# Kernel tuning notes

Measured on AMD Instinct MI355X. Metric: run time of the kernel, lower is better.

## Reference

```python
import jax, jax.numpy as jnp
import numpy as np

N_CLASSES = 18

def setup_inputs() -> dict:
    key = jax.random.key(0)
    k1, k2 = jax.random.split(key)
    B = 2_000_000
    output = jax.random.normal(k1, (B, N_CLASSES), dtype=jnp.float32)
    labels_soft = jax.random.uniform(k2, (B, N_CLASSES), dtype=jnp.float32)
    return {"output": output, "labels_soft": labels_soft}

def reference(output, labels_soft):
    # Original: sum over classes of mean_b( CE(output, cls) * labels_soft[:, cls] )
    # = mean over batch of sum_c( -log_softmax(output)[b, c] * labels_soft[b, c] )
    logp = jax.nn.log_softmax(output, axis=-1)          # [B, C]
    per_row = -jnp.sum(logp * labels_soft, axis=-1)     # [B]
    return jnp.mean(per_row)
```

## Files before the change

### kernel.cpp

```cpp
#include <hip/hip_runtime.h>

#define NCLS 18

__global__ __launch_bounds__(256) void ce_soft_kernel(
    const float* __restrict__ logits,
    const float* __restrict__ labels,
    float* __restrict__ result,
    int B, float invB)
{
    int tid = blockIdx.x * blockDim.x + threadIdx.x;
    int stride = gridDim.x * blockDim.x;

    float acc = 0.0f;
    for (int row = tid; row < B; row += stride) {
        const float2* o2 = (const float2*)(logits + (size_t)row * NCLS);
        const float2* l2 = (const float2*)(labels + (size_t)row * NCLS);
        float x[NCLS], l[NCLS];
        #pragma unroll
        for (int k = 0; k < NCLS / 2; ++k) {
            float2 v = o2[k];
            x[2 * k] = v.x; x[2 * k + 1] = v.y;
        }
        #pragma unroll
        for (int k = 0; k < NCLS / 2; ++k) {
            float2 w = l2[k];
            l[2 * k] = w.x; l[2 * k + 1] = w.y;
        }

        float m = x[0];
        #pragma unroll
        for (int c = 1; c < NCLS; ++c) m = fmaxf(m, x[c]);

        float se = 0.0f, dot = 0.0f, sl = 0.0f;
        #pragma unroll
        for (int c = 0; c < NCLS; ++c) {
            se += __expf(x[c] - m);
            dot = fmaf(l[c], x[c], dot);
            sl += l[c];
        }
        float lse = m + __logf(se);
        acc = fmaf(sl, lse, acc - dot);
    }

    #pragma unroll
    for (int off = 32; off > 0; off >>= 1)
        acc += __shfl_down(acc, off, 64);

    __shared__ float wave_sums[4];
    int lane = threadIdx.x & 63;
    int wid  = threadIdx.x >> 6;
    if (lane == 0) wave_sums[wid] = acc;
    __syncthreads();
    if (threadIdx.x == 0) {
        float s = wave_sums[0] + wave_sums[1] + wave_sums[2] + wave_sums[3];
        atomicAdd(result, s * invB);
    }
}

extern "C" void kernel_launch(void* const* d_in, const int* in_sizes, int n_in,
                              void* d_out, int out_size, void* d_ws, size_t ws_size,
                              hipStream_t stream) {
    const float* logits = (const float*)d_in[0];
    const float* labels = (const float*)d_in[1];
    float* result = (float*)d_out;

    int B = in_sizes[0] / NCLS;

    hipMemsetAsync(d_out, 0, sizeof(float), stream);

    int block = 256;
    int grid  = 2048;
    ce_soft_kernel<<<grid, block, 0, stream>>>(logits, labels, result, B, 1.0f / (float)B);
}
```

Baseline: 292.1 us.

## Stage row tiles through shared memory for coalesced global loads

Each block now copies a 256-row tile of logits and labels into LDS using contiguous float2 loads, then each thread reads its own row from shared memory to compute the log-sum-exp and dot product. This replaces the per-thread strided row reads, which were poorly coalesced. It costs 36 KB of LDS per block, which limits occupancy, and adds two barriers per tile with no overlap between load and compute.

```diff
diff --git a/kernel.cpp b/kernel.cpp
--- a/kernel.cpp
+++ b/kernel.cpp
@@ -1,45 +1,60 @@
 #include <hip/hip_runtime.h>
 
 #define NCLS 18
+#define TILE_ROWS 256
+#define TILE_F2 (TILE_ROWS * NCLS / 2)
 
 __global__ __launch_bounds__(256) void ce_soft_kernel(
-    const float* __restrict__ logits,
-    const float* __restrict__ labels,
+    const float2* __restrict__ logits2,
+    const float2* __restrict__ labels2,
     float* __restrict__ result,
     int B, float invB)
 {
-    int tid = blockIdx.x * blockDim.x + threadIdx.x;
-    int stride = gridDim.x * blockDim.x;
+    __shared__ float2 sX[TILE_F2];
+    __shared__ float2 sL[TILE_F2];
+
+    const int t = threadIdx.x;
+    const int nTiles = (B + TILE_ROWS - 1) / TILE_ROWS;
 
     float acc = 0.0f;
-    for (int row = tid; row < B; row += stride) {
-        const float2* o2 = (const float2*)(logits + (size_t)row * NCLS);
-        const float2* l2 = (const float2*)(labels + (size_t)row * NCLS);
-        float x[NCLS], l[NCLS];
-        #pragma unroll
-        for (int k = 0; k < NCLS / 2; ++k) {
-            float2 v = o2[k];
-            x[2 * k] = v.x; x[2 * k + 1] = v.y;
+    for (int tile = blockIdx.x; tile < nTiles; tile += gridDim.x) {
+        const int rowBase = tile * TILE_ROWS;
+        const int rows = min(TILE_ROWS, B - rowBase);
+        const int n2 = rows * (NCLS / 2);
+        const size_t g2 = (size_t)rowBase * (NCLS / 2);
+
+        for (int g = t; g < n2; g += 256) {
+            sX[g] = logits2[g2 + g];
+            sL[g] = labels2[g2 + g];
         }
-        #pragma unroll
-        for (int k = 0; k < NCLS / 2; ++k) {
-            float2 w = l2[k];
-            l[2 * k] = w.x; l[2 * k + 1] = w.y;
+        __syncthreads();
+
+        if (t < rows) {
+            const float2* xr = &sX[t * (NCLS / 2)];
+            const float2* lr = &sL[t * (NCLS / 2)];
+            float x[NCLS];
+            #pragma unroll
+            for (int j = 0; j < NCLS / 2; ++j) {
+                float2 v = xr[j];
+                x[2 * j] = v.x; x[2 * j + 1] = v.y;
+            }
+            float m = x[0];
+            #pragma unroll
+            for (int c = 1; c < NCLS; ++c) m = fmaxf(m, x[c]);
+
+            float se = 0.0f, dot = 0.0f, sl = 0.0f;
+            #pragma unroll
+            for (int j = 0; j < NCLS / 2; ++j) {
+                float2 w = lr[j];
+                se += __expf(x[2 * j] - m) + __expf(x[2 * j + 1] - m);
+                dot = fmaf(w.x, x[2 * j], dot);
+                dot = fmaf(w.y, x[2 * j + 1], dot);
+                sl += w.x + w.y;
+            }
+            float lse = m + __logf(se);
+            acc = fmaf(sl, lse, acc - dot);
         }
-
-        float m = x[0];
-        #pragma unroll
-        for (int c = 1; c < NCLS; ++c) m = fmaxf(m, x[c]);
-
-        float se = 0.0f, dot = 0.0f, sl = 0.0f;
-        #pragma unroll
-        for (int c = 0; c < NCLS; ++c) {
-            se += __expf(x[c] - m);
-            dot = fmaf(l[c], x[c], dot);
-            sl += l[c];
-        }
-        float lse = m + __logf(se);
-        acc = fmaf(sl, lse, acc - dot);
+        __syncthreads();
     }
 
     #pragma unroll
@@ -47,11 +62,11 @@
         acc += __shfl_down(acc, off, 64);
 
     __shared__ float wave_sums[4];
-    int lane = threadIdx.x & 63;
-    int wid  = threadIdx.x >> 6;
+    const int lane = t & 63;
+    const int wid  = t >> 6;
     if (lane == 0) wave_sums[wid] = acc;
     __syncthreads();
-    if (threadIdx.x == 0) {
+    if (t == 0) {
         float s = wave_sums[0] + wave_sums[1] + wave_sums[2] + wave_sums[3];
         atomicAdd(result, s * invB);
     }
@@ -60,8 +75,8 @@
 extern "C" void kernel_launch(void* const* d_in, const int* in_sizes, int n_in,
                               void* d_out, int out_size, void* d_ws, size_t ws_size,
                               hipStream_t stream) {
-    const float* logits = (const float*)d_in[0];
-    const float* labels = (const float*)d_in[1];
+    const float2* logits2 = (const float2*)d_in[0];
+    const float2* labels2 = (const float2*)d_in[1];
     float* result = (float*)d_out;
 
     int B = in_sizes[0] / NCLS;
@@ -70,5 +85,5 @@
 
     int block = 256;
     int grid  = 2048;
-    ce_soft_kernel<<<grid, block, 0, stream>>>(logits, labels, result, B, 1.0f / (float)B);
+    ce_soft_kernel<<<grid, block, 0, stream>>>(logits2, labels2, result, B, 1.0f / (float)B);
 }
```

Measured after the change: 302.8 us. 1.04x slower.
